# Performance work log

Measured on AMD Instinct MI355X. Metric: run time of the kernel, lower is better.

## Reference

```python
import jax, jax.numpy as jnp
import numpy as np

N, E = 40000, 640000
NODE_DIM, EDGE_DIM, H = 128, 64, 8
DK = NODE_DIM // H


def setup_inputs() -> dict:
    key = jax.random.key(0)
    ks = jax.random.split(key, 12)
    s = 1.0 / np.sqrt(NODE_DIM)
    se = 1.0 / np.sqrt(EDGE_DIM)
    return {
        "nodes": jax.random.normal(ks[0], (N, NODE_DIM), jnp.float32),
        "edge_index": jax.random.randint(ks[1], (2, E), 0, N, jnp.int64),
        "edge_attr": jax.random.normal(ks[2], (E, EDGE_DIM), jnp.float32),
        # Linear weights stored as [in, out] so y = x @ W + b
        "wq": jax.random.uniform(ks[3], (NODE_DIM, NODE_DIM), jnp.float32, -s, s),
        "bq": jnp.zeros((NODE_DIM,), jnp.float32),
        "wk": jax.random.uniform(ks[4], (NODE_DIM, NODE_DIM), jnp.float32, -s, s),
        "bk": jnp.zeros((NODE_DIM,), jnp.float32),
        "wv": jax.random.uniform(ks[5], (NODE_DIM, NODE_DIM), jnp.float32, -s, s),
        "bv": jnp.zeros((NODE_DIM,), jnp.float32),
        "we": jax.random.uniform(ks[6], (EDGE_DIM, NODE_DIM), jnp.float32, -se, se),
        "be": jnp.zeros((NODE_DIM,), jnp.float32),
        "wo": jax.random.uniform(ks[7], (NODE_DIM, NODE_DIM), jnp.float32, -s, s),
        "bo": jnp.zeros((NODE_DIM,), jnp.float32),
    }


def reference(nodes, edge_index, edge_attr, wq, bq, wk, bk, wv, bv, we, be, wo, bo):
    n = nodes.shape[0]
    inv_sqrt_dk = 1.0 / np.sqrt(DK).astype(np.float32)
    Q = (nodes @ wq + bq).reshape(n, H, DK)
    K = (nodes @ wk + bk).reshape(n, H, DK)
    V = (nodes @ wv + bv).reshape(n, H, DK)
    row, col = edge_index[0], edge_index[1]
    Qr = Q[row]                                   # [E, H, DK]
    scores = (Qr * K[col]).sum(-1) * inv_sqrt_dk  # [E, H]
    ef = (edge_attr @ we + be).reshape(-1, H, DK)
    scores = scores + (Qr * ef).sum(-1) * inv_sqrt_dk
    es = jnp.exp(scores)                          # unnormalized exp (matches torch code: no max-subtraction)
    denom = jax.ops.segment_sum(es, row, num_segments=n)       # [N, H]
    w = es / (denom[row] + 1e-8)                  # [E, H]
    msg = w[..., None] * V[col]                   # [E, H, DK]
    out = jax.ops.segment_sum(msg, row, num_segments=n).reshape(n, -1)
    return out @ wo + bo
```

## Files before the change

kernel.cpp:

```cpp
#include <hip/hip_runtime.h>
#include <hip/hip_fp16.h>

#define NN  40000
#define NE  640000
#define ND  128
#define ED  64
#define NH  8
#define DK  16
#define NWT 912

#define SCAN_NBLK 157
#define PREP_NBLK 524

typedef _Float16 f16x8 __attribute__((ext_vector_type(8)));
typedef float    f32x4 __attribute__((ext_vector_type(4)));

__global__ __launch_bounds__(256) void k_prep_hist(const float* __restrict__ wq,
                                                   const float* __restrict__ bq,
                                                   const float* __restrict__ wk,
                                                   const float* __restrict__ bk,
                                                   const float* __restrict__ wv,
                                                   const float* __restrict__ bv,
                                                   const float* __restrict__ we,
                                                   const float* __restrict__ be,
                                                   const float* __restrict__ wo,
                                                   const int* __restrict__ ei,
                                                   __half* __restrict__ WT,
                                                   __half* __restrict__ woT,
                                                   float* __restrict__ bias_all,
                                                   int* __restrict__ hist) {
  if (blockIdx.x >= PREP_NBLK) {
    const int e = (blockIdx.x - PREP_NBLK) * 256 + threadIdx.x;
    if (e < NE) atomicAdd(&hist[ei[e]], 1);
    return;
  }
  int idx = blockIdx.x * 256 + threadIdx.x;
  if (idx < NWT * ND) {
    const int n = idx >> 7, k = idx & 127;
    float v;
    if (n < 128)      v = wq[k * ND + n];
    else if (n < 256) v = wk[k * ND + (n - 128)];
    else if (n < 384) v = wv[k * ND + (n - 256)];
    else if (n < 896) {
      const int col = n - 384, h = col >> 6, j = col & 63;
      const float4* a = (const float4*)(wq + (size_t)k * ND + h * DK);
      const float4* b = (const float4*)(we + (size_t)j * ND + h * DK);
      float s = 0.f;
#pragma unroll
      for (int i = 0; i < 4; ++i) {
        float4 av = a[i], bv4 = b[i];
        s = fmaf(av.x, bv4.x, s); s = fmaf(av.y, bv4.y, s);
        s = fmaf(av.z, bv4.z, s); s = fmaf(av.w, bv4.w, s);
      }
      v = 0.25f * s;
    } else if (n < 904) {
      const int h = n - 896;
      const float4* a = (const float4*)(wq + (size_t)k * ND + h * DK);
      const float4* b = (const float4*)(be + h * DK);
      float s = 0.f;
#pragma unroll
      for (int i = 0; i < 4; ++i) {
        float4 av = a[i], bv4 = b[i];
        s = fmaf(av.x, bv4.x, s); s = fmaf(av.y, bv4.y, s);
        s = fmaf(av.z, bv4.z, s); s = fmaf(av.w, bv4.w, s);
      }
      v = 0.25f * s;
    } else v = 0.f;
    WT[idx] = __float2half_rn(v);
    return;
  }
  idx -= NWT * ND;
  if (idx < ND * ND) {
    const int n = idx >> 7, k = idx & 127;
    woT[idx] = __float2half_rn(wo[k * ND + n]);
    return;
  }
  idx -= ND * ND;
  if (idx < NWT) {
    float v;
    if (idx < 128)      v = bq[idx];
    else if (idx < 256) v = bk[idx - 128];
    else if (idx < 384) v = bv[idx - 256];
    else if (idx < 896) {
      const int col = idx - 384, h = col >> 6, j = col & 63;
      const float4* a = (const float4*)(bq + h * DK);
      const float4* b = (const float4*)(we + (size_t)j * ND + h * DK);
      float s = 0.f;
#pragma unroll
      for (int i = 0; i < 4; ++i) {
        float4 av = a[i], bv4 = b[i];
        s = fmaf(av.x, bv4.x, s); s = fmaf(av.y, bv4.y, s);
        s = fmaf(av.z, bv4.z, s); s = fmaf(av.w, bv4.w, s);
      }
      v = 0.25f * s;
    } else if (idx < 904) {
      const int h = idx - 896;
      const float4* a = (const float4*)(bq + h * DK);
      const float4* b = (const float4*)(be + h * DK);
      float s = 0.f;
#pragma unroll
      for (int i = 0; i < 4; ++i) {
        float4 av = a[i], bv4 = b[i];
        s = fmaf(av.x, bv4.x, s); s = fmaf(av.y, bv4.y, s);
        s = fmaf(av.z, bv4.z, s); s = fmaf(av.w, bv4.w, s);
      }
      v = 0.25f * s;
    } else v = 0.f;
    bias_all[idx] = v;
  }
}

__global__ __launch_bounds__(256) void k_gemm1(const float* __restrict__ x,
                                               const __half* __restrict__ WT,
                                               const float* __restrict__ bias_all,
                                               __half* __restrict__ qh,
                                               __half* __restrict__ K16,
                                               __half* __restrict__ V16,
                                               __half* __restrict__ G16,
                                               float* __restrict__ SB) {
  __shared__ _Float16 bs[4][16][132];
  const int wave = threadIdx.x >> 6;
  const int l    = threadIdx.x & 63;
  const int row  = l & 15;
  const int kq   = l >> 4;
  const int r0   = blockIdx.x * 64 + wave * 16;

  f16x8 a[4];
#pragma unroll
  for (int s = 0; s < 4; ++s) {
    const float4* ap = (const float4*)(x + (size_t)(r0 + row) * ND + s * 32 + kq * 8);
    const float4 f0 = ap[0], f1 = ap[1];
    f16x8 t;
    t[0] = (_Float16)f0.x; t[1] = (_Float16)f0.y; t[2] = (_Float16)f0.z; t[3] = (_Float16)f0.w;
    t[4] = (_Float16)f1.x; t[5] = (_Float16)f1.y; t[6] = (_Float16)f1.z; t[7] = (_Float16)f1.w;
    a[s] = t;
  }

  const int rb = r0 + kq * 4;

  for (int nc = 0; nc < 56; nc += 4) {
    __syncthreads();
    {
      const __half* src = WT + (size_t)((nc + wave) * 16 + row) * ND;
      _Float16* dst = &bs[wave][row][0];
#pragma unroll
      for (int ch = 0; ch < 4; ++ch) {
        const int o = (kq + ch * 4) * 8;
        *(f16x8*)(dst + o) = *(const f16x8*)(src + o);
      }
    }
    __syncthreads();
#pragma unroll
    for (int t = 0; t < 4; ++t) {
      const int nt = nc + t;
      f32x4 c = {0.f, 0.f, 0.f, 0.f};
#pragma unroll
      for (int s = 0; s < 4; ++s) {
        const f16x8 b = *(const f16x8*)&bs[t][row][s * 32 + kq * 8];
        c = __builtin_amdgcn_mfma_f32_16x16x32_f16(a[s], b, c, 0, 0, 0);
      }
      const int col = nt * 16 + row;
      const float bb = bias_all[col];
      if (nt < 24) {
        __half* dst = (nt < 8) ? (qh + col) : (nt < 16) ? (K16 + (col - 128)) : (V16 + (col - 256));
#pragma unroll
        for (int i = 0; i < 4; ++i)
          dst[(size_t)(rb + i) * ND] = __float2half_rn(c[i] + bb);
      } else {
        const int gcol = col - 384;
#pragma unroll
        for (int i = 0; i < 4; ++i)
          G16[(size_t)(rb + i) * 512 + gcol] = __float2half_rn(c[i] + bb);
      }
    }
  }

  {
    f32x4 c = {0.f, 0.f, 0.f, 0.f};
#pragma unroll
    for (int s = 0; s < 4; ++s) {
      const f16x8 b = *(const f16x8*)(WT + (size_t)(896 + row) * ND + s * 32 + kq * 8);
      c = __builtin_amdgcn_mfma_f32_16x16x32_f16(a[s], b, c, 0, 0, 0);
    }
    if (row < 8) {
      const float bb = bias_all[896 + row];
#pragma unroll
      for (int i = 0; i < 4; ++i)
        SB[(size_t)(rb + i) * NH + row] = c[i] + bb;
    }
  }
}

__global__ __launch_bounds__(256) void k_gemm2(const __half* __restrict__ mh,
                                               const __half* __restrict__ woT,
                                               const float* __restrict__ bo,
                                               float* __restrict__ out) {
  __shared__ _Float16 ws[128][132];
  const int tid  = threadIdx.x;
  const int wave = tid >> 6;
  const int l    = tid & 63;
  const int row  = l & 15;
  const int kq   = l >> 4;
  const int r0   = blockIdx.x * 64 + wave * 16;

  {
    const int r = tid & 127, hf = tid >> 7;
    const __half* src = woT + (size_t)r * ND + hf * 64;
    _Float16* dst = &ws[r][hf * 64];
#pragma unroll
    for (int ch = 0; ch < 8; ++ch)
      *(f16x8*)(dst + ch * 8) = *(const f16x8*)(src + ch * 8);
  }

  f16x8 a[4];
#pragma unroll
  for (int s = 0; s < 4; ++s)
    a[s] = *(const f16x8*)(mh + (size_t)(r0 + row) * ND + s * 32 + kq * 8);

  __syncthreads();

  const int rb = r0 + kq * 4;
#pragma unroll 2
  for (int nt = 0; nt < 8; ++nt) {
    f32x4 c = {0.f, 0.f, 0.f, 0.f};
#pragma unroll
    for (int s = 0; s < 4; ++s) {
      const f16x8 b = *(const f16x8*)&ws[nt * 16 + row][s * 32 + kq * 8];
      c = __builtin_amdgcn_mfma_f32_16x16x32_f16(a[s], b, c, 0, 0, 0);
    }
    const int col = nt * 16 + row;
    const float bb = bo[col];
#pragma unroll
    for (int i = 0; i < 4; ++i)
      out[(size_t)(rb + i) * ND + col] = c[i] + bb;
  }
}

__global__ __launch_bounds__(256) void k_scan1(const int* __restrict__ hist,
                                               int* __restrict__ off,
                                               int* __restrict__ bsum) {
  __shared__ int sh[256];
  const int tid = threadIdx.x;
  const int idx = blockIdx.x * 256 + tid;
  int v = (idx < NN) ? hist[idx] : 0;
  sh[tid] = v;
  __syncthreads();
#pragma unroll
  for (int d = 1; d < 256; d <<= 1) {
    int t = (tid >= d) ? sh[tid - d] : 0;
    __syncthreads();
    sh[tid] += t;
    __syncthreads();
  }
  if (idx < NN) off[idx] = sh[tid] - v;
  if (tid == 255) bsum[blockIdx.x] = sh[255];
}

__global__ __launch_bounds__(256) void k_scan2(int* __restrict__ bsum) {
  __shared__ int sh[256];
  const int tid = threadIdx.x;
  int v = (tid < SCAN_NBLK) ? bsum[tid] : 0;
  sh[tid] = v;
  __syncthreads();
#pragma unroll
  for (int d = 1; d < 256; d <<= 1) {
    int t = (tid >= d) ? sh[tid - d] : 0;
    __syncthreads();
    sh[tid] += t;
    __syncthreads();
  }
  if (tid < SCAN_NBLK) bsum[tid] = sh[tid] - v;
}

__global__ __launch_bounds__(256) void k_scan3(int* __restrict__ off,
                                               const int* __restrict__ bsum,
                                               int* __restrict__ cursor) {
  const int idx = blockIdx.x * 256 + threadIdx.x;
  if (idx < NN) {
    int o = off[idx] + bsum[blockIdx.x];
    off[idx] = o;
    cursor[idx] = o;
  }
  if (blockIdx.x == 0 && threadIdx.x == 0) off[NN] = NE;
}

__global__ __launch_bounds__(256) void k_scatter(const int* __restrict__ ei,
                                                 int* __restrict__ cursor,
                                                 int2* __restrict__ pair) {
  int e = blockIdx.x * 256 + threadIdx.x;
  if (e >= NE) return;
  int row = ei[e];
  int col = ei[NE + e];
  int pos = atomicAdd(&cursor[row], 1);
  pair[pos] = make_int2(col, e);
}

#define LOADKV(col, KA, KB, VA, VB) \
  const float2 kr##KA = *(const float2*)(K16 + (size_t)(col) * ND + hq);        \
  const float2 vr##KA = *(const float2*)(V16 + (size_t)(col) * ND + hq);        \
  float2 KA, KB, VA, VB;                                                        \
  { const __half2* _h = (const __half2*)&kr##KA;                                \
    KA = __half22float2(_h[0]); KB = __half22float2(_h[1]); }                   \
  { const __half2* _h = (const __half2*)&vr##KA;                                \
    VA = __half22float2(_h[0]); VB = __half22float2(_h[1]); }

__global__ __launch_bounds__(256) void k_gather(const __half* __restrict__ qh,
                                                const __half* __restrict__ K16,
                                                const __half* __restrict__ V16,
                                                const float* __restrict__ ea,
                                                const int* __restrict__ off,
                                                const int2* __restrict__ pair,
                                                const __half* __restrict__ G16,
                                                const float* __restrict__ SB,
                                                __half* __restrict__ mh) {
  __shared__ float eas[8][8 * ED];
  const int g = threadIdx.x >> 5;
  const int n = blockIdx.x * 8 + g;
  const int l = threadIdx.x & 31;
  const int h = l >> 2;
  const int q = l & 3;

  float gg[16];
  float4 qv;
  {
    const __half2* qp2 = (const __half2*)(qh + (size_t)n * ND + h * DK + q * 4);
    float2 q01 = __half22float2(qp2[0]);
    float2 q23 = __half22float2(qp2[1]);
    qv.x = q01.x * 0.25f; qv.y = q01.y * 0.25f;
    qv.z = q23.x * 0.25f; qv.w = q23.y * 0.25f;
  }
  const float sb = SB[n * NH + h];
  {
    const float4* gp = (const float4*)(G16 + (size_t)n * 512 + h * 64 + q * 16);
    float4 c0 = gp[0], c1 = gp[1];
    const __half2* h0 = (const __half2*)&c0;
    const __half2* h1 = (const __half2*)&c1;
#pragma unroll
    for (int i = 0; i < 4; ++i) {
      float2 f0 = __half22float2(h0[i]);
      gg[2 * i + 0] = f0.x; gg[2 * i + 1] = f0.y;
      float2 f1 = __half22float2(h1[i]);
      gg[8 + 2 * i + 0] = f1.x; gg[8 + 2 * i + 1] = f1.y;
    }
  }

  float4 acc = make_float4(0.f, 0.f, 0.f, 0.f);
  float den = 0.f;

  const int j0 = off[n], j1 = off[n + 1];
  const int jlast = j1 - 1;
  const int hq = h * DK + q * 4;
  const int l8 = l & 7;
  const int se = l >> 2;
  const int sp = l & 3;

  if (j0 < j1) {
    int2 p = pair[min(j0 + l8, jlast)];
    float4 er0, er1, er2, er3;
    {
      const int eid = __shfl(p.y, se, 32);
      const float4* s4 = (const float4*)(ea + (size_t)eid * ED) + sp;
      er0 = s4[0]; er1 = s4[4]; er2 = s4[8]; er3 = s4[12];
    }
    int2 pn = pair[min(j0 + 8 + l8, jlast)];

    for (int jp = j0; jp < j1; jp += 8) {
      {
        float* d = &eas[g][se * ED] + sp * 4;
        *(float4*)(d + 0)  = er0; *(float4*)(d + 16) = er1;
        *(float4*)(d + 32) = er2; *(float4*)(d + 48) = er3;
      }
      int2 pf = pn;
      if (jp + 8 < j1) {
        const int eidN = __shfl(pn.y, se, 32);
        const float4* s4 = (const float4*)(ea + (size_t)eidN * ED) + sp;
        er0 = s4[0]; er1 = s4[4]; er2 = s4[8]; er3 = s4[12];
        pf = pair[min(jp + 16 + l8, jlast)];
      }
      asm volatile("s_waitcnt lgkmcnt(0)" ::: "memory");
      __builtin_amdgcn_sched_barrier(0);

#pragma unroll
      for (int cb = 0; cb < 8; cb += 4) {
        const int col0 = __shfl(p.x, cb + 0, 32);
        const int col1 = __shfl(p.x, cb + 1, 32);
        const int col2 = __shfl(p.x, cb + 2, 32);
        const int col3 = __shfl(p.x, cb + 3, 32);

        LOADKV(col0, ka0, kb0, va0, vb0);
        LOADKV(col1, ka1, kb1, va1, vb1);
        LOADKV(col2, ka2, kb2, va2, vb2);
        LOADKV(col3, ka3, kb3, va3, vb3);

        float s0 = ka0.x * qv.x; s0 = fmaf(qv.y, ka0.y, s0); s0 = fmaf(qv.z, kb0.x, s0); s0 = fmaf(qv.w, kb0.y, s0);
        float s1 = ka1.x * qv.x; s1 = fmaf(qv.y, ka1.y, s1); s1 = fmaf(qv.z, kb1.x, s1); s1 = fmaf(qv.w, kb1.y, s1);
        float s2 = ka2.x * qv.x; s2 = fmaf(qv.y, ka2.y, s2); s2 = fmaf(qv.z, kb2.x, s2); s2 = fmaf(qv.w, kb2.y, s2);
        float s3 = ka3.x * qv.x; s3 = fmaf(qv.y, ka3.y, s3); s3 = fmaf(qv.z, kb3.x, s3); s3 = fmaf(qv.w, kb3.y, s3);

        const float4* e0 = (const float4*)&eas[g][(cb + 0) * ED + q * 16];
        const float4* e1 = (const float4*)&eas[g][(cb + 1) * ED + q * 16];
        const float4* e2 = (const float4*)&eas[g][(cb + 2) * ED + q * 16];
        const float4* e3 = (const float4*)&eas[g][(cb + 3) * ED + q * 16];
#pragma unroll
        for (int i = 0; i < 4; ++i) {
          float4 a = e0[i];
          s0 = fmaf(a.x, gg[4 * i + 0], s0); s0 = fmaf(a.y, gg[4 * i + 1], s0);
          s0 = fmaf(a.z, gg[4 * i + 2], s0); s0 = fmaf(a.w, gg[4 * i + 3], s0);
        }
#pragma unroll
        for (int i = 0; i < 4; ++i) {
          float4 a = e1[i];
          s1 = fmaf(a.x, gg[4 * i + 0], s1); s1 = fmaf(a.y, gg[4 * i + 1], s1);
          s1 = fmaf(a.z, gg[4 * i + 2], s1); s1 = fmaf(a.w, gg[4 * i + 3], s1);
        }
#pragma unroll
        for (int i = 0; i < 4; ++i) {
          float4 a = e2[i];
          s2 = fmaf(a.x, gg[4 * i + 0], s2); s2 = fmaf(a.y, gg[4 * i + 1], s2);
          s2 = fmaf(a.z, gg[4 * i + 2], s2); s2 = fmaf(a.w, gg[4 * i + 3], s2);
        }
#pragma unroll
        for (int i = 0; i < 4; ++i) {
          float4 a = e3[i];
          s3 = fmaf(a.x, gg[4 * i + 0], s3); s3 = fmaf(a.y, gg[4 * i + 1], s3);
          s3 = fmaf(a.z, gg[4 * i + 2], s3); s3 = fmaf(a.w, gg[4 * i + 3], s3);
        }

        s0 += __shfl_xor(s0, 1); s0 += __shfl_xor(s0, 2);
        s1 += __shfl_xor(s1, 1); s1 += __shfl_xor(s1, 2);
        s2 += __shfl_xor(s2, 1); s2 += __shfl_xor(s2, 2);
        s3 += __shfl_xor(s3, 1); s3 += __shfl_xor(s3, 2);

        const float es0 = (jp + cb + 0 < j1) ? __expf(s0 + sb) : 0.f;
        const float es1 = (jp + cb + 1 < j1) ? __expf(s1 + sb) : 0.f;
        const float es2 = (jp + cb + 2 < j1) ? __expf(s2 + sb) : 0.f;
        const float es3 = (jp + cb + 3 < j1) ? __expf(s3 + sb) : 0.f;
        den += (es0 + es1) + (es2 + es3);

        acc.x = fmaf(es0, va0.x, acc.x); acc.y = fmaf(es0, va0.y, acc.y);
        acc.z = fmaf(es0, vb0.x, acc.z); acc.w = fmaf(es0, vb0.y, acc.w);
        acc.x = fmaf(es1, va1.x, acc.x); acc.y = fmaf(es1, va1.y, acc.y);
        acc.z = fmaf(es1, vb1.x, acc.z); acc.w = fmaf(es1, vb1.y, acc.w);
        acc.x = fmaf(es2, va2.x, acc.x); acc.y = fmaf(es2, va2.y, acc.y);
        acc.z = fmaf(es2, vb2.x, acc.z); acc.w = fmaf(es2, vb2.y, acc.w);
        acc.x = fmaf(es3, va3.x, acc.x); acc.y = fmaf(es3, va3.y, acc.y);
        acc.z = fmaf(es3, vb3.x, acc.z); acc.w = fmaf(es3, vb3.y, acc.w);
      }

      p = pn; pn = pf;
    }
  }

  const float inv = 1.f / (den + 1e-8f);
  union { __half2 h2[2]; float2 f; } u;
  u.h2[0] = __floats2half2_rn(acc.x * inv, acc.y * inv);
  u.h2[1] = __floats2half2_rn(acc.z * inv, acc.w * inv);
  *(float2*)(mh + (size_t)n * ND + h * DK + q * 4) = u.f;
}

extern "C" void kernel_launch(void* const* d_in, const int* in_sizes, int n_in,
                              void* d_out, int out_size, void* d_ws, size_t ws_size,
                              hipStream_t stream) {
  const float* nodes = (const float*)d_in[0];
  const int*   ei    = (const int*)d_in[1];
  const float* ea    = (const float*)d_in[2];
  const float* wq    = (const float*)d_in[3];
  const float* bq    = (const float*)d_in[4];
  const float* wk    = (const float*)d_in[5];
  const float* bk    = (const float*)d_in[6];
  const float* wv    = (const float*)d_in[7];
  const float* bv    = (const float*)d_in[8];
  const float* we    = (const float*)d_in[9];
  const float* be    = (const float*)d_in[10];
  const float* wo    = (const float*)d_in[11];
  const float* bo    = (const float*)d_in[12];
  float* out = (float*)d_out;

  const size_t NND = (size_t)NN * ND;
  __half* qh   = (__half*)d_ws;
  __half* K16  = qh + NND;
  __half* V16  = K16 + NND;
  __half* mh   = V16 + NND;
  __half* G16  = mh + NND;
  __half* WT   = G16 + (size_t)NN * 512;
  __half* woT  = WT + (size_t)NWT * ND;
  float* SB    = (float*)(woT + ND * ND);
  float* bias_all = SB + (size_t)NN * NH;
  int* hist    = (int*)(bias_all + NWT);
  int* off     = hist + NN;
  int* cursor  = off + 40004;
  int* bsum    = cursor + NN;
  int2* pair   = (int2*)(bsum + 256);

  hipMemsetAsync(hist, 0, NN * sizeof(int), stream);

  dim3 blk(256);

  k_prep_hist<<<dim3(PREP_NBLK + (NE + 255) / 256), blk, 0, stream>>>(
      wq, bq, wk, bk, wv, bv, we, be, wo, ei, WT, woT, bias_all, hist);

  k_gemm1<<<dim3(NN / 64), blk, 0, stream>>>(nodes, WT, bias_all, qh, K16, V16, G16, SB);

  k_scan1<<<dim3(SCAN_NBLK), blk, 0, stream>>>(hist, off, bsum);
  k_scan2<<<dim3(1), blk, 0, stream>>>(bsum);
  k_scan3<<<dim3(SCAN_NBLK), blk, 0, stream>>>(off, bsum, cursor);
  dim3 gE((NE + 255) / 256);
  k_scatter<<<gE, blk, 0, stream>>>(ei, cursor, pair);

  k_gather<<<dim3(NN / 8), blk, 0, stream>>>(qh, K16, V16, ea, off, pair, G16, SB, mh);

  k_gemm2<<<dim3(NN / 64), blk, 0, stream>>>(mh, woT, bo, out);
}
```

Before: 211.1 us.

## Use persistent wave-per-node gather with atomic work queue and direct edge-attr loads

The gather kernel becomes persistent: 1024 blocks fetch node indices from a global atomic counter, one 64-lane wave per node. Each half-wave handles four of the eight edges in a chunk, and the two halves' partial sums are combined with cross-half shuffles. Edge attributes are now read straight from global memory instead of being staged through shared memory with the software prefetch pipeline. This aims to balance uneven node degrees and fill the full wave width, at the cost of an atomic per node and losing the explicit edge-attribute prefetch.

```diff
diff --git a/kernel.cpp b/kernel.cpp
--- a/kernel.cpp
+++ b/kernel.cpp
@@ -304,6 +304,22 @@
   { const __half2* _h = (const __half2*)&vr##KA;                                \
     VA = __half22float2(_h[0]); VB = __half22float2(_h[1]); }
 
+#define EA_ACC(sc, EP) do {                                                    \
+  float4 _a;                                                                   \
+  _a = (EP)[0];                                                                \
+  sc = fmaf(_a.x, gg[0], sc);  sc = fmaf(_a.y, gg[1], sc);                     \
+  sc = fmaf(_a.z, gg[2], sc);  sc = fmaf(_a.w, gg[3], sc);                     \
+  _a = (EP)[1];                                                                \
+  sc = fmaf(_a.x, gg[4], sc);  sc = fmaf(_a.y, gg[5], sc);                     \
+  sc = fmaf(_a.z, gg[6], sc);  sc = fmaf(_a.w, gg[7], sc);                     \
+  _a = (EP)[2];                                                                \
+  sc = fmaf(_a.x, gg[8], sc);  sc = fmaf(_a.y, gg[9], sc);                     \
+  sc = fmaf(_a.z, gg[10], sc); sc = fmaf(_a.w, gg[11], sc);                    \
+  _a = (EP)[3];                                                                \
+  sc = fmaf(_a.x, gg[12], sc); sc = fmaf(_a.y, gg[13], sc);                    \
+  sc = fmaf(_a.z, gg[14], sc); sc = fmaf(_a.w, gg[15], sc);                    \
+} while (0)
+
 __global__ __launch_bounds__(256) void k_gather(const __half* __restrict__ qh,
                                                 const __half* __restrict__ K16,
                                                 const __half* __restrict__ V16,
@@ -312,129 +328,93 @@
                                                 const int2* __restrict__ pair,
                                                 const __half* __restrict__ G16,
                                                 const float* __restrict__ SB,
+                                                int* __restrict__ nctr,
                                                 __half* __restrict__ mh) {
-  __shared__ float eas[8][8 * ED];
-  const int g = threadIdx.x >> 5;
-  const int n = blockIdx.x * 8 + g;
-  const int l = threadIdx.x & 31;
-  const int h = l >> 2;
-  const int q = l & 3;
-
-  float gg[16];
-  float4 qv;
-  {
-    const __half2* qp2 = (const __half2*)(qh + (size_t)n * ND + h * DK + q * 4);
-    float2 q01 = __half22float2(qp2[0]);
-    float2 q23 = __half22float2(qp2[1]);
-    qv.x = q01.x * 0.25f; qv.y = q01.y * 0.25f;
-    qv.z = q23.x * 0.25f; qv.w = q23.y * 0.25f;
-  }
-  const float sb = SB[n * NH + h];
-  {
-    const float4* gp = (const float4*)(G16 + (size_t)n * 512 + h * 64 + q * 16);
-    float4 c0 = gp[0], c1 = gp[1];
-    const __half2* h0 = (const __half2*)&c0;
-    const __half2* h1 = (const __half2*)&c1;
-#pragma unroll
-    for (int i = 0; i < 4; ++i) {
-      float2 f0 = __half22float2(h0[i]);
-      gg[2 * i + 0] = f0.x; gg[2 * i + 1] = f0.y;
-      float2 f1 = __half22float2(h1[i]);
-      gg[8 + 2 * i + 0] = f1.x; gg[8 + 2 * i + 1] = f1.y;
-    }
-  }
-
-  float4 acc = make_float4(0.f, 0.f, 0.f, 0.f);
-  float den = 0.f;
-
-  const int j0 = off[n], j1 = off[n + 1];
-  const int jlast = j1 - 1;
+  const int l  = threadIdx.x & 63;
+  const int e2 = l >> 5;
+  const int h  = (l >> 2) & 7;
+  const int q  = l & 3;
   const int hq = h * DK + q * 4;
   const int l8 = l & 7;
-  const int se = l >> 2;
-  const int sp = l & 3;
-
-  if (j0 < j1) {
-    int2 p = pair[min(j0 + l8, jlast)];
-    float4 er0, er1, er2, er3;
+
+  for (;;) {
+    int n;
+    if (l == 0) n = atomicAdd(nctr, 1);
+    n = __shfl(n, 0, 64);
+    if (n >= NN) break;
+
+    float gg[16];
+    float4 qv;
     {
-      const int eid = __shfl(p.y, se, 32);
-      const float4* s4 = (const float4*)(ea + (size_t)eid * ED) + sp;
-      er0 = s4[0]; er1 = s4[4]; er2 = s4[8]; er3 = s4[12];
-    }
-    int2 pn = pair[min(j0 + 8 + l8, jlast)];
-
-    for (int jp = j0; jp < j1; jp += 8) {
-      {
-        float* d = &eas[g][se * ED] + sp * 4;
-        *(float4*)(d + 0)  = er0; *(float4*)(d + 16) = er1;
-        *(float4*)(d + 32) = er2; *(float4*)(d + 48) = er3;
-      }
-      int2 pf = pn;
-      if (jp + 8 < j1) {
-        const int eidN = __shfl(pn.y, se, 32);
-        const float4* s4 = (const float4*)(ea + (size_t)eidN * ED) + sp;
-        er0 = s4[0]; er1 = s4[4]; er2 = s4[8]; er3 = s4[12];
-        pf = pair[min(jp + 16 + l8, jlast)];
-      }
-      asm volatile("s_waitcnt lgkmcnt(0)" ::: "memory");
-      __builtin_amdgcn_sched_barrier(0);
-
-#pragma unroll
-      for (int cb = 0; cb < 8; cb += 4) {
-        const int col0 = __shfl(p.x, cb + 0, 32);
-        const int col1 = __shfl(p.x, cb + 1, 32);
-        const int col2 = __shfl(p.x, cb + 2, 32);
-        const int col3 = __shfl(p.x, cb + 3, 32);
+      const __half2* qp2 = (const __half2*)(qh + (size_t)n * ND + hq);
+      float2 q01 = __half22float2(qp2[0]);
+      float2 q23 = __half22float2(qp2[1]);
+      qv.x = q01.x * 0.25f; qv.y = q01.y * 0.25f;
+      qv.z = q23.x * 0.25f; qv.w = q23.y * 0.25f;
+    }
+    const float sb = SB[n * NH + h];
+    {
+      const float4* gp = (const float4*)(G16 + (size_t)n * 512 + h * 64 + q * 16);
+      float4 c0 = gp[0], c1 = gp[1];
+      const __half2* h0 = (const __half2*)&c0;
+      const __half2* h1 = (const __half2*)&c1;
+#pragma unroll
+      for (int i = 0; i < 4; ++i) {
+        float2 f0 = __half22float2(h0[i]);
+        gg[2 * i + 0] = f0.x; gg[2 * i + 1] = f0.y;
+        float2 f1 = __half22float2(h1[i]);
+        gg[8 + 2 * i + 0] = f1.x; gg[8 + 2 * i + 1] = f1.y;
+      }
+    }
+
+    float4 acc = make_float4(0.f, 0.f, 0.f, 0.f);
+    float den = 0.f;
+
+    const int j0 = off[n], j1 = off[n + 1];
+    const int jlast = j1 - 1;
+
+    if (j0 < j1) {
+      int2 p = pair[min(j0 + l8, jlast)];
+      for (int jp = j0; jp < j1; jp += 8) {
+        const int2 pn = pair[min(jp + 8 + l8, jlast)];
+
+        const int eb = e2 * 4;
+        const int col0 = __shfl(p.x, eb + 0, 32);
+        const int col1 = __shfl(p.x, eb + 1, 32);
+        const int col2 = __shfl(p.x, eb + 2, 32);
+        const int col3 = __shfl(p.x, eb + 3, 32);
+        const int eid0 = __shfl(p.y, eb + 0, 32);
+        const int eid1 = __shfl(p.y, eb + 1, 32);
+        const int eid2 = __shfl(p.y, eb + 2, 32);
+        const int eid3 = __shfl(p.y, eb + 3, 32);
 
         LOADKV(col0, ka0, kb0, va0, vb0);
         LOADKV(col1, ka1, kb1, va1, vb1);
         LOADKV(col2, ka2, kb2, va2, vb2);
         LOADKV(col3, ka3, kb3, va3, vb3);
 
+        const float4* E0 = (const float4*)(ea + (size_t)eid0 * ED + q * 16);
+        const float4* E1 = (const float4*)(ea + (size_t)eid1 * ED + q * 16);
+        const float4* E2 = (const float4*)(ea + (size_t)eid2 * ED + q * 16);
+        const float4* E3 = (const float4*)(ea + (size_t)eid3 * ED + q * 16);
+
         float s0 = ka0.x * qv.x; s0 = fmaf(qv.y, ka0.y, s0); s0 = fmaf(qv.z, kb0.x, s0); s0 = fmaf(qv.w, kb0.y, s0);
         float s1 = ka1.x * qv.x; s1 = fmaf(qv.y, ka1.y, s1); s1 = fmaf(qv.z, kb1.x, s1); s1 = fmaf(qv.w, kb1.y, s1);
         float s2 = ka2.x * qv.x; s2 = fmaf(qv.y, ka2.y, s2); s2 = fmaf(qv.z, kb2.x, s2); s2 = fmaf(qv.w, kb2.y, s2);
         float s3 = ka3.x * qv.x; s3 = fmaf(qv.y, ka3.y, s3); s3 = fmaf(qv.z, kb3.x, s3); s3 = fmaf(qv.w, kb3.y, s3);
 
-        const float4* e0 = (const float4*)&eas[g][(cb + 0) * ED + q * 16];
-        const float4* e1 = (const float4*)&eas[g][(cb + 1) * ED + q * 16];
-        const float4* e2 = (const float4*)&eas[g][(cb + 2) * ED + q * 16];
-        const float4* e3 = (const float4*)&eas[g][(cb + 3) * ED + q * 16];
-#pragma unroll
-        for (int i = 0; i < 4; ++i) {
-          float4 a = e0[i];
-          s0 = fmaf(a.x, gg[4 * i + 0], s0); s0 = fmaf(a.y, gg[4 * i + 1], s0);
-          s0 = fmaf(a.z, gg[4 * i + 2], s0); s0 = fmaf(a.w, gg[4 * i + 3], s0);
-        }
-#pragma unroll
-        for (int i = 0; i < 4; ++i) {
-          float4 a = e1[i];
-          s1 = fmaf(a.x, gg[4 * i + 0], s1); s1 = fmaf(a.y, gg[4 * i + 1], s1);
-          s1 = fmaf(a.z, gg[4 * i + 2], s1); s1 = fmaf(a.w, gg[4 * i + 3], s1);
-        }
-#pragma unroll
-        for (int i = 0; i < 4; ++i) {
-          float4 a = e2[i];
-          s2 = fmaf(a.x, gg[4 * i + 0], s2); s2 = fmaf(a.y, gg[4 * i + 1], s2);
-          s2 = fmaf(a.z, gg[4 * i + 2], s2); s2 = fmaf(a.w, gg[4 * i + 3], s2);
-        }
-#pragma unroll
-        for (int i = 0; i < 4; ++i) {
-          float4 a = e3[i];
-          s3 = fmaf(a.x, gg[4 * i + 0], s3); s3 = fmaf(a.y, gg[4 * i + 1], s3);
-          s3 = fmaf(a.z, gg[4 * i + 2], s3); s3 = fmaf(a.w, gg[4 * i + 3], s3);
-        }
+        EA_ACC(s0, E0); EA_ACC(s1, E1); EA_ACC(s2, E2); EA_ACC(s3, E3);
 
         s0 += __shfl_xor(s0, 1); s0 += __shfl_xor(s0, 2);
         s1 += __shfl_xor(s1, 1); s1 += __shfl_xor(s1, 2);
         s2 += __shfl_xor(s2, 1); s2 += __shfl_xor(s2, 2);
         s3 += __shfl_xor(s3, 1); s3 += __shfl_xor(s3, 2);
 
-        const float es0 = (jp + cb + 0 < j1) ? __expf(s0 + sb) : 0.f;
-        const float es1 = (jp + cb + 1 < j1) ? __expf(s1 + sb) : 0.f;
-        const float es2 = (jp + cb + 2 < j1) ? __expf(s2 + sb) : 0.f;
-        const float es3 = (jp + cb + 3 < j1) ? __expf(s3 + sb) : 0.f;
+        const int ebase = jp + eb;
+        const float es0 = (ebase + 0 < j1) ? __expf(s0 + sb) : 0.f;
+        const float es1 = (ebase + 1 < j1) ? __expf(s1 + sb) : 0.f;
+        const float es2 = (ebase + 2 < j1) ? __expf(s2 + sb) : 0.f;
+        const float es3 = (ebase + 3 < j1) ? __expf(s3 + sb) : 0.f;
         den += (es0 + es1) + (es2 + es3);
 
         acc.x = fmaf(es0, va0.x, acc.x); acc.y = fmaf(es0, va0.y, acc.y);
@@ -445,17 +425,25 @@
         acc.z = fmaf(es2, vb2.x, acc.z); acc.w = fmaf(es2, vb2.y, acc.w);
         acc.x = fmaf(es3, va3.x, acc.x); acc.y = fmaf(es3, va3.y, acc.y);
         acc.z = fmaf(es3, vb3.x, acc.z); acc.w = fmaf(es3, vb3.y, acc.w);
-      }
-
-      p = pn; pn = pf;
-    }
-  }
-
-  const float inv = 1.f / (den + 1e-8f);
-  union { __half2 h2[2]; float2 f; } u;
-  u.h2[0] = __floats2half2_rn(acc.x * inv, acc.y * inv);
-  u.h2[1] = __floats2half2_rn(acc.z * inv, acc.w * inv);
-  *(float2*)(mh + (size_t)n * ND + h * DK + q * 4) = u.f;
+
+        p = pn;
+      }
+    }
+
+    den   += __shfl_xor(den, 32);
+    acc.x += __shfl_xor(acc.x, 32);
+    acc.y += __shfl_xor(acc.y, 32);
+    acc.z += __shfl_xor(acc.z, 32);
+    acc.w += __shfl_xor(acc.w, 32);
+
+    if (e2 == 0) {
+      const float inv = 1.f / (den + 1e-8f);
+      union { __half2 h2[2]; float2 f; } u;
+      u.h2[0] = __floats2half2_rn(acc.x * inv, acc.y * inv);
+      u.h2[1] = __floats2half2_rn(acc.z * inv, acc.w * inv);
+      *(float2*)(mh + (size_t)n * ND + hq) = u.f;
+    }
+  }
 }
 
 extern "C" void kernel_launch(void* const* d_in, const int* in_sizes, int n_in,
@@ -490,9 +478,11 @@
   int* off     = hist + NN;
   int* cursor  = off + 40004;
   int* bsum    = cursor + NN;
-  int2* pair   = (int2*)(bsum + 256);
+  int* nctr    = bsum + 256;
+  int2* pair   = (int2*)(nctr + 4);
 
   hipMemsetAsync(hist, 0, NN * sizeof(int), stream);
+  hipMemsetAsync(nctr, 0, sizeof(int), stream);
 
   dim3 blk(256);
 
@@ -507,7 +497,7 @@
   dim3 gE((NE + 255) / 256);
   k_scatter<<<gE, blk, 0, stream>>>(ei, cursor, pair);
 
-  k_gather<<<dim3(NN / 8), blk, 0, stream>>>(qh, K16, V16, ea, off, pair, G16, SB, mh);
+  k_gather<<<dim3(1024), blk, 0, stream>>>(qh, K16, V16, ea, off, pair, G16, SB, nctr, mh);
 
   k_gemm2<<<dim3(NN / 64), blk, 0, stream>>>(mh, woT, bo, out);
 }
```

After: 666.8 us. 3.16x slower.

## Process each node with a full wavefront splitting edges across half-waves

Applied to the files above, without the earlier changes.

The gather kernel now assigns one 64-lane wavefront per node instead of one 32-lane half. Each half processes a different group of 8 edges, so each loop iteration covers 16 edges, and partial sums are combined with a cross-half shuffle at the end. This aims to cut per-node loop iterations and latency chains at typical degrees. In exchange it doubles the number of wavefronts, duplicates per-node setup loads, and wastes more lanes on low-degree tails.

```diff
diff --git a/kernel.cpp b/kernel.cpp
--- a/kernel.cpp
+++ b/kernel.cpp
@@ -313,17 +313,22 @@
                                                 const __half* __restrict__ G16,
                                                 const float* __restrict__ SB,
                                                 __half* __restrict__ mh) {
-  __shared__ float eas[8][8 * ED];
-  const int g = threadIdx.x >> 5;
-  const int n = blockIdx.x * 8 + g;
-  const int l = threadIdx.x & 31;
-  const int h = l >> 2;
-  const int q = l & 3;
+  __shared__ float eas[4][16 * ED];
+  const int w  = threadIdx.x >> 6;
+  const int n  = blockIdx.x * 4 + w;
+  const int l  = threadIdx.x & 63;
+  const int e2 = l >> 5;
+  const int h  = (l >> 2) & 7;
+  const int q  = l & 3;
+  const int hq = h * DK + q * 4;
+  const int l16 = l & 15;
+  const int se  = l >> 2;
+  const int sp  = l & 3;
 
   float gg[16];
   float4 qv;
   {
-    const __half2* qp2 = (const __half2*)(qh + (size_t)n * ND + h * DK + q * 4);
+    const __half2* qp2 = (const __half2*)(qh + (size_t)n * ND + hq);
     float2 q01 = __half22float2(qp2[0]);
     float2 q23 = __half22float2(qp2[1]);
     qv.x = q01.x * 0.25f; qv.y = q01.y * 0.25f;
@@ -349,43 +354,40 @@
 
   const int j0 = off[n], j1 = off[n + 1];
   const int jlast = j1 - 1;
-  const int hq = h * DK + q * 4;
-  const int l8 = l & 7;
-  const int se = l >> 2;
-  const int sp = l & 3;
 
   if (j0 < j1) {
-    int2 p = pair[min(j0 + l8, jlast)];
+    int2 p = pair[min(j0 + l16, jlast)];
     float4 er0, er1, er2, er3;
     {
-      const int eid = __shfl(p.y, se, 32);
+      const int eid = __shfl(p.y, se, 64);
       const float4* s4 = (const float4*)(ea + (size_t)eid * ED) + sp;
       er0 = s4[0]; er1 = s4[4]; er2 = s4[8]; er3 = s4[12];
     }
-    int2 pn = pair[min(j0 + 8 + l8, jlast)];
-
-    for (int jp = j0; jp < j1; jp += 8) {
+    int2 pn = pair[min(j0 + 16 + l16, jlast)];
+
+    for (int jp = j0; jp < j1; jp += 16) {
       {
-        float* d = &eas[g][se * ED] + sp * 4;
+        float* d = &eas[w][se * ED] + sp * 4;
         *(float4*)(d + 0)  = er0; *(float4*)(d + 16) = er1;
         *(float4*)(d + 32) = er2; *(float4*)(d + 48) = er3;
       }
       int2 pf = pn;
-      if (jp + 8 < j1) {
-        const int eidN = __shfl(pn.y, se, 32);
+      if (jp + 16 < j1) {
+        const int eidN = __shfl(pn.y, se, 64);
         const float4* s4 = (const float4*)(ea + (size_t)eidN * ED) + sp;
         er0 = s4[0]; er1 = s4[4]; er2 = s4[8]; er3 = s4[12];
-        pf = pair[min(jp + 16 + l8, jlast)];
+        pf = pair[min(jp + 32 + l16, jlast)];
       }
       asm volatile("s_waitcnt lgkmcnt(0)" ::: "memory");
       __builtin_amdgcn_sched_barrier(0);
 
+      const int eb = e2 * 8;
 #pragma unroll
       for (int cb = 0; cb < 8; cb += 4) {
-        const int col0 = __shfl(p.x, cb + 0, 32);
-        const int col1 = __shfl(p.x, cb + 1, 32);
-        const int col2 = __shfl(p.x, cb + 2, 32);
-        const int col3 = __shfl(p.x, cb + 3, 32);
+        const int col0 = __shfl(p.x, eb + cb + 0, 64);
+        const int col1 = __shfl(p.x, eb + cb + 1, 64);
+        const int col2 = __shfl(p.x, eb + cb + 2, 64);
+        const int col3 = __shfl(p.x, eb + cb + 3, 64);
 
         LOADKV(col0, ka0, kb0, va0, vb0);
         LOADKV(col1, ka1, kb1, va1, vb1);
@@ -397,10 +399,10 @@
         float s2 = ka2.x * qv.x; s2 = fmaf(qv.y, ka2.y, s2); s2 = fmaf(qv.z, kb2.x, s2); s2 = fmaf(qv.w, kb2.y, s2);
         float s3 = ka3.x * qv.x; s3 = fmaf(qv.y, ka3.y, s3); s3 = fmaf(qv.z, kb3.x, s3); s3 = fmaf(qv.w, kb3.y, s3);
 
-        const float4* e0 = (const float4*)&eas[g][(cb + 0) * ED + q * 16];
-        const float4* e1 = (const float4*)&eas[g][(cb + 1) * ED + q * 16];
-        const float4* e2 = (const float4*)&eas[g][(cb + 2) * ED + q * 16];
-        const float4* e3 = (const float4*)&eas[g][(cb + 3) * ED + q * 16];
+        const float4* e0 = (const float4*)&eas[w][(eb + cb + 0) * ED + q * 16];
+        const float4* e1 = (const float4*)&eas[w][(eb + cb + 1) * ED + q * 16];
+        const float4* e2p = (const float4*)&eas[w][(eb + cb + 2) * ED + q * 16];
+        const float4* e3 = (const float4*)&eas[w][(eb + cb + 3) * ED + q * 16];
 #pragma unroll
         for (int i = 0; i < 4; ++i) {
           float4 a = e0[i];
@@ -415,7 +417,7 @@
         }
 #pragma unroll
         for (int i = 0; i < 4; ++i) {
-          float4 a = e2[i];
+          float4 a = e2p[i];
           s2 = fmaf(a.x, gg[4 * i + 0], s2); s2 = fmaf(a.y, gg[4 * i + 1], s2);
           s2 = fmaf(a.z, gg[4 * i + 2], s2); s2 = fmaf(a.w, gg[4 * i + 3], s2);
         }
@@ -431,10 +433,11 @@
         s2 += __shfl_xor(s2, 1); s2 += __shfl_xor(s2, 2);
         s3 += __shfl_xor(s3, 1); s3 += __shfl_xor(s3, 2);
 
-        const float es0 = (jp + cb + 0 < j1) ? __expf(s0 + sb) : 0.f;
-        const float es1 = (jp + cb + 1 < j1) ? __expf(s1 + sb) : 0.f;
-        const float es2 = (jp + cb + 2 < j1) ? __expf(s2 + sb) : 0.f;
-        const float es3 = (jp + cb + 3 < j1) ? __expf(s3 + sb) : 0.f;
+        const int ebase = jp + eb + cb;
+        const float es0 = (ebase + 0 < j1) ? __expf(s0 + sb) : 0.f;
+        const float es1 = (ebase + 1 < j1) ? __expf(s1 + sb) : 0.f;
+        const float es2 = (ebase + 2 < j1) ? __expf(s2 + sb) : 0.f;
+        const float es3 = (ebase + 3 < j1) ? __expf(s3 + sb) : 0.f;
         den += (es0 + es1) + (es2 + es3);
 
         acc.x = fmaf(es0, va0.x, acc.x); acc.y = fmaf(es0, va0.y, acc.y);
@@ -451,11 +454,19 @@
     }
   }
 
-  const float inv = 1.f / (den + 1e-8f);
-  union { __half2 h2[2]; float2 f; } u;
-  u.h2[0] = __floats2half2_rn(acc.x * inv, acc.y * inv);
-  u.h2[1] = __floats2half2_rn(acc.z * inv, acc.w * inv);
-  *(float2*)(mh + (size_t)n * ND + h * DK + q * 4) = u.f;
+  den   += __shfl_xor(den, 32);
+  acc.x += __shfl_xor(acc.x, 32);
+  acc.y += __shfl_xor(acc.y, 32);
+  acc.z += __shfl_xor(acc.z, 32);
+  acc.w += __shfl_xor(acc.w, 32);
+
+  if (e2 == 0) {
+    const float inv = 1.f / (den + 1e-8f);
+    union { __half2 h2[2]; float2 f; } u;
+    u.h2[0] = __floats2half2_rn(acc.x * inv, acc.y * inv);
+    u.h2[1] = __floats2half2_rn(acc.z * inv, acc.w * inv);
+    *(float2*)(mh + (size_t)n * ND + hq) = u.f;
+  }
 }
 
 extern "C" void kernel_launch(void* const* d_in, const int* in_sizes, int n_in,
@@ -507,7 +518,7 @@
   dim3 gE((NE + 255) / 256);
   k_scatter<<<gE, blk, 0, stream>>>(ei, cursor, pair);
 
-  k_gather<<<dim3(NN / 8), blk, 0, stream>>>(qh, K16, V16, ea, off, pair, G16, SB, mh);
+  k_gather<<<dim3(NN / 4), blk, 0, stream>>>(qh, K16, V16, ea, off, pair, G16, SB, mh);
 
   k_gemm2<<<dim3(NN / 64), blk, 0, stream>>>(mh, woT, bo, out);
 }
```

After: 226.2 us. 7.1% more time.
